# Optimization experiments

Hardware: AMD Instinct MI355X
Metric: run time of the kernel (lower is better)

## Reference

```python
import jax, jax.numpy as jnp
import numpy as np

TYPE_N = 5
EPS = 1e-6  # torch F.pairwise_distance default eps, added to the difference before the norm


def setup_inputs() -> dict:
    key = jax.random.key(0)
    k1, k2 = jax.random.split(key)
    N, D = 200000, 256
    x = jax.random.normal(k1, (N, D), dtype=jnp.float32)
    y_real = jax.random.normal(k2, (N, TYPE_N), dtype=jnp.float32)
    return {"x": x, "y_real": y_real}


def reference(x, y_real):
    xf = x.reshape(x.shape[0], -1)                      # [N, D]
    labels = jnp.argmax(y_real, axis=1)                 # [N]
    dt = xf.dtype

    # per-class counts and centroid sums (segment reduce, one pass)
    counts = jax.ops.segment_sum(jnp.ones((xf.shape[0],), dt), labels, num_segments=TYPE_N)  # [C]
    sums = jax.ops.segment_sum(xf, labels, num_segments=TYPE_N)                              # [C, D]
    safe_counts = jnp.maximum(counts, 1.0)
    center = jnp.where(counts[:, None] > 0, sums / safe_counts[:, None], 0.0)                # [C, D]

    # positive loss: mean intra-class distance to centroid, summed over present classes
    d = jnp.linalg.norm(xf - center[labels] + EPS, axis=1)                                   # [N]
    per_class_mean = jax.ops.segment_sum(d, labels, num_segments=TYPE_N) / safe_counts       # [C]
    present = (counts > 0) & (jnp.sum(center, axis=1) != 0)                                  # [C]
    loss_pos = jnp.sum(jnp.where(present, per_class_mean, 0.0))
    real_n = jnp.sum(present.astype(dt))

    # negative loss: mean pairwise distance between present centers (C is tiny)
    diff = center[:, None, :] - center[None, :, :] + EPS                                     # [C, C, D]
    pd = jnp.linalg.norm(diff, axis=-1)                                                      # [C, C]
    triu = jnp.triu(jnp.ones((TYPE_N, TYPE_N), bool), k=1)
    pair_mask = triu & present[:, None] & present[None, :]
    n_pairs = real_n * (real_n - 1.0) / 2.0
    loss_neg = jnp.where(real_n > 1,
                         jnp.sum(jnp.where(pair_mask, pd, 0.0)) / jnp.maximum(n_pairs, 1.0),
                         0.0)

    loss_pos = jnp.where(real_n > 0, loss_pos / jnp.maximum(real_n, 1.0), 1.0)
    return loss_pos / (loss_neg + loss_pos)
```

## Files before the change

kernel.cpp:

```cpp
#include <hip/hip_runtime.h>
#include <math.h>

#define TYPE_N 5
#define D 256
#define EPS 1e-6f
#define NCOPY 16

#define OFF_CNTP   (NCOPY * TYPE_N * D)
#define OFF_CENTER (OFF_CNTP + NCOPY * TYPE_N)
#define OFF_CNTF   (OFF_CENTER + TYPE_N * D)
#define OFF_DSUM   (OFF_CNTF + TYPE_N)
#define OFF_CME    (OFF_DSUM + NCOPY * TYPE_N)
#define WS_FLOATS  (OFF_CME + TYPE_N * D)

__device__ __forceinline__ int argmax5(const float* __restrict__ yr) {
    int lab = 0;
    float best = yr[0];
    #pragma unroll
    for (int c = 1; c < TYPE_N; ++c) {
        float v = yr[c];
        if (v > best) { best = v; lab = c; }
    }
    return lab;
}

__device__ __forceinline__ int row_label(const float* __restrict__ y, int r, int lane) {
    int lab = 0;
    if (lane == 0) {
        const float* yr = y + (size_t)r * TYPE_N;
        float best = yr[0];
        #pragma unroll
        for (int c = 1; c < TYPE_N; ++c) {
            float v = yr[c];
            if (v > best) { best = v; lab = c; }
        }
    }
    return __shfl(lab, 0);
}

__global__ __launch_bounds__(256) void k1_sums(const float* __restrict__ x,
                                               const float* __restrict__ y,
                                               float* __restrict__ ws, int N) {
    __shared__ float lsum[4][TYPE_N][D];
    __shared__ float lcnt[4][TYPE_N];
    const int lane = threadIdx.x & 63;
    const int wid  = threadIdx.x >> 6;
    float acc[TYPE_N][4] = {};
    float cnt[TYPE_N] = {};
    const float cw = (lane == 0) ? 1.0f : 0.0f;
    const int stride = gridDim.x * 4;
    for (int r = blockIdx.x * 4 + wid; r < N; r += stride) {
        int lab = row_label(y, r, lane);
        const float4 v = *reinterpret_cast<const float4*>(x + (size_t)r * D + lane * 4);
        #pragma unroll
        for (int c = 0; c < TYPE_N; ++c) {
            float m = (lab == c) ? 1.0f : 0.0f;
            acc[c][0] = fmaf(m, v.x, acc[c][0]);
            acc[c][1] = fmaf(m, v.y, acc[c][1]);
            acc[c][2] = fmaf(m, v.z, acc[c][2]);
            acc[c][3] = fmaf(m, v.w, acc[c][3]);
            cnt[c]    = fmaf(m, cw, cnt[c]);
        }
    }
    #pragma unroll
    for (int c = 0; c < TYPE_N; ++c) {
        *reinterpret_cast<float4*>(&lsum[wid][c][lane * 4]) =
            make_float4(acc[c][0], acc[c][1], acc[c][2], acc[c][3]);
        if (lane == 0) lcnt[wid][c] = cnt[c];
    }
    __syncthreads();
    const int t = threadIdx.x;
    float* sums = ws + (size_t)(blockIdx.x % NCOPY) * (TYPE_N * D);
    #pragma unroll
    for (int c = 0; c < TYPE_N; ++c) {
        float s = lsum[0][c][t] + lsum[1][c][t] + lsum[2][c][t] + lsum[3][c][t];
        atomicAdd(&sums[c * D + t], s);
    }
    if (t < TYPE_N) {
        float s = lcnt[0][t] + lcnt[1][t] + lcnt[2][t] + lcnt[3][t];
        atomicAdd(&ws[OFF_CNTP + (blockIdx.x % NCOPY) * TYPE_N + t], s);
    }
}

__global__ __launch_bounds__(256) void k2_center(float* __restrict__ ws) {
    const int t = threadIdx.x;
    float cnts[TYPE_N];
    #pragma unroll
    for (int c = 0; c < TYPE_N; ++c) {
        float s = 0.f;
        #pragma unroll
        for (int p = 0; p < NCOPY; ++p) s += ws[OFF_CNTP + p * TYPE_N + c];
        cnts[c] = s;
    }
    float* center = ws + OFF_CENTER;
    float* cme    = ws + OFF_CME;
    #pragma unroll
    for (int c = 0; c < TYPE_N; ++c) {
        float s = 0.f;
        #pragma unroll
        for (int p = 0; p < NCOPY; ++p) s += ws[p * TYPE_N * D + c * D + t];
        float sc = fmaxf(cnts[c], 1.0f);
        float ctr = (cnts[c] > 0.f) ? s / sc : 0.f;
        center[c * D + t] = ctr;
        cme[c * D + t]    = ctr - EPS;
    }
    if (t < TYPE_N) ws[OFF_CNTF + t] = cnts[t];
}

__global__ __launch_bounds__(256) void k3_dist(const float* __restrict__ x,
                                               const float* __restrict__ y,
                                               float* __restrict__ ws, int N) {
    __shared__ float lds[4][TYPE_N];
    const int lane = threadIdx.x & 63;
    const int wid  = threadIdx.x >> 6;
    const int r = blockIdx.x * 256 + threadIdx.x;

    int lab = 0;
    float d = 0.f;
    if (r < N) {
        lab = argmax5(y + (size_t)r * TYPE_N);
        const float4* xr = reinterpret_cast<const float4*>(x + (size_t)r * D);
        const float4* cr = reinterpret_cast<const float4*>(ws + OFF_CME + lab * D);
        float ss[4] = {0.f, 0.f, 0.f, 0.f};
        #pragma unroll 8
        for (int i = 0; i < 64; ++i) {
            const float4 a = xr[i];
            const float4 b = cr[i];
            const float t0 = a.x - b.x;
            const float t1 = a.y - b.y;
            const float t2 = a.z - b.z;
            const float t3 = a.w - b.w;
            float s = fmaf(t0, t0, t1 * t1);
            s = fmaf(t2, t2, s);
            s = fmaf(t3, t3, s);
            ss[i & 3] += s;
        }
        d = sqrtf(ss[0] + ss[1] + ss[2] + ss[3]);
    }

    #pragma unroll
    for (int c = 0; c < TYPE_N; ++c) {
        float v = (lab == c) ? d : 0.f;
        #pragma unroll
        for (int off = 32; off > 0; off >>= 1) v += __shfl_xor(v, off);
        if (lane == 0) lds[wid][c] = v;
    }
    __syncthreads();
    if (threadIdx.x < TYPE_N) {
        float s = lds[0][threadIdx.x] + lds[1][threadIdx.x] +
                  lds[2][threadIdx.x] + lds[3][threadIdx.x];
        atomicAdd(&ws[OFF_DSUM + (blockIdx.x % NCOPY) * TYPE_N + threadIdx.x], s);
    }
}

__global__ __launch_bounds__(64) void k4_final(const float* __restrict__ ws,
                                               float* __restrict__ out) {
    const int lane = threadIdx.x;
    const float* center = ws + OFF_CENTER;
    const float* counts = ws + OFF_CNTF;
    const float* dsp    = ws + OFF_DSUM;

    float csum[TYPE_N];
    #pragma unroll
    for (int c = 0; c < TYPE_N; ++c) {
        float s = 0.f;
        #pragma unroll
        for (int k = 0; k < 4; ++k) s += center[c * D + lane * 4 + k];
        #pragma unroll
        for (int off = 32; off > 0; off >>= 1) s += __shfl_xor(s, off);
        csum[c] = s;
    }

    float cnts[TYPE_N], dsum[TYPE_N];
    bool present[TYPE_N];
    float real_n = 0.f;
    #pragma unroll
    for (int c = 0; c < TYPE_N; ++c) {
        cnts[c] = counts[c];
        float s = 0.f;
        #pragma unroll
        for (int p = 0; p < NCOPY; ++p) s += dsp[p * TYPE_N + c];
        dsum[c] = s;
        present[c] = (cnts[c] > 0.f) && (csum[c] != 0.f);
        real_n += present[c] ? 1.f : 0.f;
    }

    float loss_pos = 0.f;
    #pragma unroll
    for (int c = 0; c < TYPE_N; ++c) {
        float pcm = dsum[c] / fmaxf(cnts[c], 1.f);
        loss_pos += present[c] ? pcm : 0.f;
    }
    loss_pos = (real_n > 0.f) ? loss_pos / fmaxf(real_n, 1.f) : 1.0f;

    float pairsum = 0.f;
    #pragma unroll
    for (int i = 0; i < TYPE_N; ++i) {
        #pragma unroll
        for (int j = i + 1; j < TYPE_N; ++j) {
            float s = 0.f;
            #pragma unroll
            for (int k = 0; k < 4; ++k) {
                float dd = center[i * D + lane * 4 + k] - center[j * D + lane * 4 + k] + EPS;
                s += dd * dd;
            }
            #pragma unroll
            for (int off = 32; off > 0; off >>= 1) s += __shfl_xor(s, off);
            float pd = sqrtf(s);
            pairsum += (present[i] && present[j]) ? pd : 0.f;
        }
    }
    float n_pairs = real_n * (real_n - 1.f) * 0.5f;
    float loss_neg = (real_n > 1.f) ? pairsum / fmaxf(n_pairs, 1.f) : 0.f;

    if (lane == 0) out[0] = loss_pos / (loss_neg + loss_pos);
}

extern "C" void kernel_launch(void* const* d_in, const int* in_sizes, int n_in,
                              void* d_out, int out_size, void* d_ws, size_t ws_size,
                              hipStream_t stream) {
    const float* x = (const float*)d_in[0];
    const float* y = (const float*)d_in[1];
    float* out = (float*)d_out;
    float* ws  = (float*)d_ws;
    const int N = in_sizes[0] / D;

    hipMemsetAsync(d_ws, 0, (size_t)WS_FLOATS * sizeof(float), stream);

    k1_sums<<<2048, 256, 0, stream>>>(x, y, ws, N);
    k2_center<<<1, 256, 0, stream>>>(ws);
    const int grid3 = (N + 255) / 256;
    k3_dist<<<grid3, 256, 0, stream>>>(x, y, ws, N);
    k4_final<<<1, 64, 0, stream>>>(ws, out);
}
```

Baseline: 124.7 us.

## Give k1 contiguous row chunks per block and compute labels without shuffles

k1_sums changes from a grid-strided loop over 2048 blocks to 2000 blocks, each handling a contiguous chunk of 100 rows. Each wave computes the argmax labels for all four rows of a group directly, with no lane-0 compute plus __shfl broadcast, and then selects its own row's label. The aim is better locality for x and y and a shorter dependency chain per row. In exchange every lane repeats 4x5 label loads, and the number of blocks issuing atomics into the 16 copies is about the same.

Result: faster. 115.2 us (-7.6%).

```diff
diff --git a/kernel.cpp b/kernel.cpp
--- a/kernel.cpp
+++ b/kernel.cpp
@@ -5,6 +5,7 @@
 #define D 256
 #define EPS 1e-6f
 #define NCOPY 16
+#define RPB 100
 
 #define OFF_CNTP   (NCOPY * TYPE_N * D)
 #define OFF_CENTER (OFF_CNTP + NCOPY * TYPE_N)
@@ -24,37 +25,36 @@
     return lab;
 }
 
-__device__ __forceinline__ int row_label(const float* __restrict__ y, int r, int lane) {
-    int lab = 0;
-    if (lane == 0) {
-        const float* yr = y + (size_t)r * TYPE_N;
-        float best = yr[0];
-        #pragma unroll
-        for (int c = 1; c < TYPE_N; ++c) {
-            float v = yr[c];
-            if (v > best) { best = v; lab = c; }
-        }
-    }
-    return __shfl(lab, 0);
-}
-
 __global__ __launch_bounds__(256) void k1_sums(const float* __restrict__ x,
                                                const float* __restrict__ y,
                                                float* __restrict__ ws, int N) {
     __shared__ float lsum[4][TYPE_N][D];
     __shared__ float lcnt[4][TYPE_N];
     const int lane = threadIdx.x & 63;
-    const int wid  = threadIdx.x >> 6;
+    const int sub  = threadIdx.x >> 6;
+    const int r0   = blockIdx.x * RPB;
+    const int rows = (N - r0 < RPB) ? (N - r0) : RPB;
+
     float acc[TYPE_N][4] = {};
     float cnt[TYPE_N] = {};
     const float cw = (lane == 0) ? 1.0f : 0.0f;
-    const int stride = gridDim.x * 4;
-    for (int r = blockIdx.x * 4 + wid; r < N; r += stride) {
-        int lab = row_label(y, r, lane);
-        const float4 v = *reinterpret_cast<const float4*>(x + (size_t)r * D + lane * 4);
+
+    const int ng = rows >> 2;
+    for (int i = 0; i < ng; ++i) {
+        const int rb = r0 + i * 4;
+        const int lab0 = argmax5(y + (size_t)rb * TYPE_N);
+        const int lab1 = argmax5(y + (size_t)(rb + 1) * TYPE_N);
+        const int lab2 = argmax5(y + (size_t)(rb + 2) * TYPE_N);
+        const int lab3 = argmax5(y + (size_t)(rb + 3) * TYPE_N);
+        int lab = lab0;
+        lab = (sub == 1) ? lab1 : lab;
+        lab = (sub == 2) ? lab2 : lab;
+        lab = (sub == 3) ? lab3 : lab;
+        const float4 v = *reinterpret_cast<const float4*>(
+            x + (size_t)(rb + sub) * D + lane * 4);
         #pragma unroll
         for (int c = 0; c < TYPE_N; ++c) {
-            float m = (lab == c) ? 1.0f : 0.0f;
+            const float m = (lab == c) ? 1.0f : 0.0f;
             acc[c][0] = fmaf(m, v.x, acc[c][0]);
             acc[c][1] = fmaf(m, v.y, acc[c][1]);
             acc[c][2] = fmaf(m, v.z, acc[c][2]);
@@ -62,11 +62,26 @@
             cnt[c]    = fmaf(m, cw, cnt[c]);
         }
     }
-    #pragma unroll
-    for (int c = 0; c < TYPE_N; ++c) {
-        *reinterpret_cast<float4*>(&lsum[wid][c][lane * 4]) =
+    for (int r = r0 + (ng << 2) + sub; r < r0 + rows; r += 4) {
+        const int lab = argmax5(y + (size_t)r * TYPE_N);
+        const float4 v = *reinterpret_cast<const float4*>(
+            x + (size_t)r * D + lane * 4);
+        #pragma unroll
+        for (int c = 0; c < TYPE_N; ++c) {
+            const float m = (lab == c) ? 1.0f : 0.0f;
+            acc[c][0] = fmaf(m, v.x, acc[c][0]);
+            acc[c][1] = fmaf(m, v.y, acc[c][1]);
+            acc[c][2] = fmaf(m, v.z, acc[c][2]);
+            acc[c][3] = fmaf(m, v.w, acc[c][3]);
+            cnt[c]    = fmaf(m, cw, cnt[c]);
+        }
+    }
+
+    #pragma unroll
+    for (int c = 0; c < TYPE_N; ++c) {
+        *reinterpret_cast<float4*>(&lsum[sub][c][lane * 4]) =
             make_float4(acc[c][0], acc[c][1], acc[c][2], acc[c][3]);
-        if (lane == 0) lcnt[wid][c] = cnt[c];
+        if (lane == 0) lcnt[sub][c] = cnt[c];
     }
     __syncthreads();
     const int t = threadIdx.x;
@@ -225,9 +240,10 @@
     float* ws  = (float*)d_ws;
     const int N = in_sizes[0] / D;
 
-    hipMemsetAsync(d_ws, 0, (size_t)WS_FLOATS * sizeof(float), stream);
-
-    k1_sums<<<2048, 256, 0, stream>>>(x, y, ws, N);
+    (void)hipMemsetAsync(d_ws, 0, (size_t)WS_FLOATS * sizeof(float), stream);
+
+    const int grid1 = (N + RPB - 1) / RPB;
+    k1_sums<<<grid1, 256, 0, stream>>>(x, y, ws, N);
     k2_center<<<1, 256, 0, stream>>>(ws);
     const int grid3 = (N + 255) / 256;
     k3_dist<<<grid3, 256, 0, stream>>>(x, y, ws, N);
```
